# Kernel tuning notes

Measured on AMD Instinct MI355X. Metric: run time of the kernel, lower is better.

## Reference

```python
import jax, jax.numpy as jnp
import numpy as np

STRIDES = (8, 16, 32, 64, 128)
TOPK = 1000          # fixed candidate count (jit-friendly stand-in for boolean masking)
SCORE_TH = 0.05      # from `score > 0.05` in postProcessing
IOU_TH = 0.5         # standard FCOS NMS threshold


def _decode_level(cls, cnt, reg, stride):
    # cls [B,C,H,W], cnt [B,1,H,W], reg [B,4,H,W]
    B, C, H, W = cls.shape
    p_cls = jax.nn.sigmoid(cls).transpose(0, 2, 3, 1).reshape(B, H * W, C)
    p_cnt = jax.nn.sigmoid(cnt).transpose(0, 2, 3, 1).reshape(B, H * W, 1)
    p_reg = jnp.exp(reg).transpose(0, 2, 3, 1).reshape(B, H * W, 4)  # (l,t,r,b) distances
    ys = (jnp.arange(H, dtype=cls.dtype) + 0.5) * stride
    xs = (jnp.arange(W, dtype=cls.dtype) + 0.5) * stride
    yy, xx = jnp.meshgrid(ys, xs, indexing='ij')
    cx = xx.reshape(-1)[None, :]  # [1,HW]
    cy = yy.reshape(-1)[None, :]
    boxes = jnp.stack([cx - p_reg[..., 0], cy - p_reg[..., 1],
                       cx + p_reg[..., 2], cy + p_reg[..., 3]], axis=-1)  # [B,HW,4]
    return p_cls, p_cnt, boxes


def _iou_matrix(b):
    # b [K,4] (x1,y1,x2,y2) -> [K,K]
    area = jnp.clip(b[:, 2] - b[:, 0], 0) * jnp.clip(b[:, 3] - b[:, 1], 0)
    x1 = jnp.maximum(b[:, None, 0], b[None, :, 0])
    y1 = jnp.maximum(b[:, None, 1], b[None, :, 1])
    x2 = jnp.minimum(b[:, None, 2], b[None, :, 2])
    y2 = jnp.minimum(b[:, None, 3], b[None, :, 3])
    inter = jnp.clip(x2 - x1, 0) * jnp.clip(y2 - y1, 0)
    return inter / (area[:, None] + area[None, :] - inter + 1e-9)


def _nms_keep(boxes, scores):
    # boxes [K,4] sorted by descending score, scores [K] -> keep mask [K]
    K = boxes.shape[0]
    iou = _iou_matrix(boxes)
    idx = jnp.arange(K)
    keep0 = scores > SCORE_TH
    def body(i, keep):
        sup = (iou[i] > IOU_TH) & (idx > i) & keep[i]
        return keep & ~sup
    return jax.lax.fori_loop(0, K, body, keep0)


def _detect(levels):
    cls_l, cnt_l, box_l = [], [], []
    for (c, n, r), s in zip(levels, STRIDES):
        pc, pn, pb = _decode_level(c, n, r, s)
        cls_l.append(pc); cnt_l.append(pn); box_l.append(pb)
    cls = jnp.concatenate(cls_l, 1)    # [B,N,C]
    boxes = jnp.concatenate(box_l, 1)  # [B,N,4]
    score = cls.max(-1)                # per original: score from cls (cnt unused in score)
    kind = cls.argmax(-1)
    top_s, top_i = jax.lax.top_k(score, TOPK)                      # [B,K]
    top_b = jnp.take_along_axis(boxes, top_i[..., None], axis=1)   # [B,K,4]
    top_k = jnp.take_along_axis(kind, top_i, axis=1)               # [B,K]
    keep = jax.vmap(_nms_keep)(top_b, top_s)                       # [B,K] bool
    out = jnp.concatenate([top_b,
                           top_k[..., None].astype(cls.dtype),
                           top_s[..., None],
                           keep[..., None].astype(cls.dtype)], axis=-1)  # [B,K,7]
    return out


def setup_inputs() -> dict:
    key = jax.random.key(0)
    B, C = 16, 20
    hw = [(128, 160), (64, 80), (32, 40), (16, 20), (8, 10)]
    names = []
    for p in (3, 4, 5, 6, 7):
        names += [f'cls_p{p}', f'cnt_p{p}', f'reg_p{p}']
    ks = jax.random.split(key, len(names))
    inp = {}
    for li, (H, W) in enumerate(hw):
        inp[f'cls_p{li+3}'] = jax.random.normal(ks[3*li+0], (B, C, H, W), jnp.float32)
        inp[f'cnt_p{li+3}'] = jax.random.normal(ks[3*li+1], (B, 1, H, W), jnp.float32)
        inp[f'reg_p{li+3}'] = jax.random.normal(ks[3*li+2], (B, 4, H, W), jnp.float32)
    return inp


def reference(cls_p3, cnt_p3, reg_p3, cls_p4, cnt_p4, reg_p4,
              cls_p5, cnt_p5, reg_p5, cls_p6, cnt_p6, reg_p6,
              cls_p7, cnt_p7, reg_p7):
    levels = [(cls_p3, cnt_p3, reg_p3), (cls_p4, cnt_p4, reg_p4),
              (cls_p5, cnt_p5, reg_p5), (cls_p6, cnt_p6, reg_p6),
              (cls_p7, cnt_p7, reg_p7)]
    return _detect(levels)
```

## Files before the change

### kernel.cpp

```cpp
#include <hip/hip_runtime.h>
#include <math.h>

#define BATCH 16
#define NCH 20
#define NPOS 27280
#define NTOP 1000
#define KW 16
#define NBIN 4096
#define CANDCAP 4096

typedef unsigned long long u64;
typedef unsigned int u32;

__device__ __align__(16) u32 g_sb[BATCH * NPOS];
__device__ unsigned char g_kind[BATCH * NPOS];
__device__ float4 g_box[BATCH * NTOP];
__device__ float g_score[BATCH * NTOP];
__device__ u64 g_mask[BATCH * NTOP * KW];
__device__ unsigned char g_rowsup[BATCH * NTOP];

__device__ __forceinline__ int digit_of(u32 sb) {
  int d = ((int)sb - 0x3F000000) >> 11;
  return d < 0 ? 0 : (d > (NBIN - 1) ? (NBIN - 1) : d);
}

__device__ __forceinline__ int jj(int j) { return j + (j >> 6); }
#define SKEWCAP (NTOP + NTOP / 64 + 1)

__global__ __launch_bounds__(256) void k1_score(
    const float* __restrict__ c3, const float* __restrict__ c4,
    const float* __restrict__ c5, const float* __restrict__ c6,
    const float* __restrict__ c7) {
  int gid = blockIdx.x * 256 + threadIdx.x;
  if (gid >= BATCH * (NPOS / 4)) return;
  int b = gid / (NPOS / 4);
  int n0 = (gid - b * (NPOS / 4)) * 4;
  const float* cls; int off, hw;
  if (n0 < 20480)      { cls = c3; off = 0;     hw = 20480; }
  else if (n0 < 25600) { cls = c4; off = 20480; hw = 5120;  }
  else if (n0 < 26880) { cls = c5; off = 25600; hw = 1280;  }
  else if (n0 < 27200) { cls = c6; off = 26880; hw = 320;   }
  else                 { cls = c7; off = 27200; hw = 80;    }
  int local = n0 - off;
  const float4* p = (const float4*)(cls + (size_t)b * NCH * hw + local);
  int s4 = hw >> 2;
  float4 best = p[0];
  int k0 = 0, k1 = 0, k2 = 0, k3 = 0;
  for (int c = 1; c < NCH; ++c) {
    float4 v = p[(size_t)c * s4];
    if (v.x > best.x) { best.x = v.x; k0 = c; }
    if (v.y > best.y) { best.y = v.y; k1 = c; }
    if (v.z > best.z) { best.z = v.z; k2 = c; }
    if (v.w > best.w) { best.w = v.w; k3 = c; }
  }
  uint4 sb4;
  float bb[4] = {best.x, best.y, best.z, best.w};
  u32 sb[4];
#pragma unroll
  for (int i = 0; i < 4; ++i) {
    float e = (float)exp(-(double)bb[i]);
    float s = 1.0f / (1.0f + e);
    sb[i] = __float_as_uint(s);
  }
  sb4.x = sb[0]; sb4.y = sb[1]; sb4.z = sb[2]; sb4.w = sb[3];
  *(uint4*)&g_sb[(size_t)b * NPOS + n0] = sb4;
  u32 kind4 = (u32)k0 | ((u32)k1 << 8) | ((u32)k2 << 16) | ((u32)k3 << 24);
  *(u32*)&g_kind[(size_t)b * NPOS + n0] = kind4;
}

__global__ __launch_bounds__(1024) void k2_select(
    const float* __restrict__ r3, const float* __restrict__ r4,
    const float* __restrict__ r5, const float* __restrict__ r6,
    const float* __restrict__ r7, float* __restrict__ out) {
  int b = blockIdx.x;
  int tid = threadIdx.x;
  int lane = tid & 63, wid = tid >> 6;
  const u32* sbs = g_sb + (size_t)b * NPOS;

  __shared__ u32 arr[NBIN];
  __shared__ u32 suf[NBIN];
  __shared__ u64 scand[CANDCAP];
  __shared__ u32 wsum[16];
  __shared__ int sh_thr, sh_ncand;

  for (int j = tid; j < NBIN; j += 1024) arr[j] = 0;
  __syncthreads();

  for (int i = 0; i < 27; ++i) {
    int n = tid + i * 1024;
    if (n < NPOS) atomicAdd(&arr[digit_of(sbs[n])], 1u);
  }
  __syncthreads();

  {
    u32 c[4];
#pragma unroll
    for (int k = 0; k < 4; ++k) { c[k] = arr[4 * tid + k]; arr[4 * tid + k] = 0; }
    u32 tot = c[0] + c[1] + c[2] + c[3];
    u32 s = tot;
#pragma unroll
    for (int off = 1; off < 64; off <<= 1) {
      u32 v = __shfl_down(s, off);
      if (lane + off < 64) s += v;
    }
    if (lane == 0) wsum[wid] = s;
    __syncthreads();
    u32 wexcl = 0;
    for (int w2 = wid + 1; w2 < 16; ++w2) wexcl += wsum[w2];
    u32 e = wexcl + (s - tot);
    u32 e3 = e;
    u32 e2 = e3 + c[3];
    u32 e1 = e2 + c[2];
    u32 e0 = e1 + c[1];
    suf[4 * tid + 3] = e3;
    suf[4 * tid + 2] = e2;
    suf[4 * tid + 1] = e1;
    suf[4 * tid + 0] = e0;
    if (e3 < NTOP && NTOP <= e3 + c[3]) { sh_thr = 4 * tid + 3; sh_ncand = (int)(e3 + c[3]); }
    if (e2 < NTOP && NTOP <= e2 + c[2]) { sh_thr = 4 * tid + 2; sh_ncand = (int)(e2 + c[2]); }
    if (e1 < NTOP && NTOP <= e1 + c[1]) { sh_thr = 4 * tid + 1; sh_ncand = (int)(e1 + c[1]); }
    if (e0 < NTOP && NTOP <= e0 + c[0]) { sh_thr = 4 * tid + 0; sh_ncand = (int)(e0 + c[0]); }
  }
  __syncthreads();
  int thr = sh_thr;
  int Ncand = sh_ncand < CANDCAP ? sh_ncand : CANDCAP;

  for (int i = 0; i < 27; ++i) {
    int n = tid + i * 1024;
    if (n < NPOS) {
      u32 sb = sbs[n];
      int d = digit_of(sb);
      if (d >= thr) {
        u32 slot = suf[d] + atomicAdd(&arr[d], 1u);
        if (slot < CANDCAP) scand[slot] = ((u64)sb << 15) | (u32)(NPOS - n);
      }
    }
  }
  __syncthreads();

  for (int i = tid; i < Ncand; i += 1024) {
    u64 k = scand[i];
    int d = digit_of((u32)(k >> 15));
    u32 gs = suf[d];
    u32 ge = (d > 0) ? suf[d - 1] : (u32)NPOS;
    if (ge > (u32)Ncand) ge = (u32)Ncand;
    int rank = (int)gs;
    for (u32 j = gs; j < ge; ++j) rank += (int)(scand[j] > k);
    if (rank >= NTOP) continue;
    u32 n = (u32)NPOS - (u32)(k & 0x7FFFu);
    float sc = __uint_as_float((u32)(k >> 15));
    const float* reg; int off, hw, lvl;
    if (n < 20480)      { reg = r3; off = 0;     hw = 20480; lvl = 0; }
    else if (n < 25600) { reg = r4; off = 20480; hw = 5120;  lvl = 1; }
    else if (n < 26880) { reg = r5; off = 25600; hw = 1280;  lvl = 2; }
    else if (n < 27200) { reg = r6; off = 26880; hw = 320;   lvl = 3; }
    else                { reg = r7; off = 27200; hw = 80;    lvl = 4; }
    int local = (int)n - off;
    int W = 160 >> lvl;
    int hh = local / W, ww = local - hh * W;
    float stride = (float)(8 << lvl);
    const float* rp = reg + (size_t)b * 4 * hw + local;
    float e0 = expf(rp[0]);
    float e1 = expf(rp[(size_t)hw]);
    float e2 = expf(rp[(size_t)2 * hw]);
    float e3 = expf(rp[(size_t)3 * hw]);
    float cx = (ww + 0.5f) * stride, cy = (hh + 0.5f) * stride;
    float x1 = cx - e0, y1 = cy - e1, x2 = cx + e2, y2 = cy + e3;
    int ok = b * NTOP + rank;
    g_box[ok] = make_float4(x1, y1, x2, y2);
    g_score[ok] = sc;
    float* o = out + (size_t)ok * 7;
    o[0] = x1; o[1] = y1; o[2] = x2; o[3] = y2;
    o[4] = (float)g_kind[(size_t)b * NPOS + n];
    o[5] = sc;
  }
}

__global__ __launch_bounds__(256) void k3_mask() {
  int b = blockIdx.y;
  int ig = blockIdx.x;
  int tid = threadIdx.x;
  int lane = tid & 63;
  __shared__ float4 shbox[SKEWCAP];
  __shared__ float shA[SKEWCAP];
  const float4* boxes = g_box + b * NTOP;
  for (int j = tid; j < NTOP; j += 256) {
    float4 bj = boxes[j];
    shbox[jj(j)] = bj;
    shA[jj(j)] = fmaxf(bj.z - bj.x, 0.f) * fmaxf(bj.w - bj.y, 0.f);
  }
  __syncthreads();
  int i = ig * 16 + (tid >> 4);
  int t = tid & 15;
  u64 word = 0;
  if (i < NTOP) {
    float4 bi = shbox[jj(i)];
    float aarea = shA[jj(i)];
    int j0 = t * 64;
    int jbeg = (j0 > i + 1) ? j0 : i + 1;
    int jend = (j0 + 64 < NTOP) ? j0 + 64 : NTOP;
    for (int j = jbeg; j < jend; ++j) {
      float4 bj = shbox[jj(j)];
      float barea = shA[jj(j)];
      float ix1 = fmaxf(bi.x, bj.x), iy1 = fmaxf(bi.y, bj.y);
      float ix2 = fminf(bi.z, bj.z), iy2 = fminf(bi.w, bj.w);
      float inter = fmaxf(ix2 - ix1, 0.f) * fmaxf(iy2 - iy1, 0.f);
      if (inter + inter > aarea + barea - inter + 1e-9f)
        word |= 1ull << (j - j0);
    }
    g_mask[((size_t)b * NTOP + i) * KW + t] = word;
  }
  u64 b16 = __ballot(word != 0);
  int rg = lane >> 4;
  if (t == 0 && i < NTOP)
    g_rowsup[b * NTOP + i] = (unsigned char)(((b16 >> (rg * 16)) & 0xFFFFull) ? 1 : 0);
}

__global__ __launch_bounds__(64) void k4_greedy(float* __restrict__ out) {
  int b = blockIdx.x;
  int lane = threadIdx.x;
  int col = lane & 15, g = lane >> 4;
  const u64* mask = g_mask + (size_t)b * NTOP * KW;

  u64 mdiag[KW];
  float s[KW];
  unsigned char rs[KW];
#pragma unroll
  for (int w = 0; w < KW; ++w) {
    int k = w * 64 + lane;
    mdiag[w] = (k < NTOP) ? mask[(size_t)k * KW + w] : 0ull;
    s[w] = (k < NTOP) ? g_score[b * NTOP + k] : 0.f;
    rs[w] = (k < NTOP) ? g_rowsup[b * NTOP + k] : (unsigned char)0;
  }

  u64 remv = 0;
  for (int w = 0; w < KW; ++w) {
    int k = w * 64 + lane;
    u64 keep0 = __ballot(k < NTOP && s[w] > 0.05f);
    u64 gate = __ballot(rs[w] != 0);
    u64 cur = keep0 & ~__shfl(remv, w);
    u64 rem = cur & gate;
    u64 acc = 0;
    while (rem) {
      int i = __ffsll(rem) - 1;
      u64 v = __shfl(mdiag[w], i);
      rem &= ~(v | (1ull << i));
      cur &= ~v;
      acc |= (1ull << i);
    }
    u64 upd = 0;
#pragma unroll
    for (int r = 0; r < 16; ++r) {
      int i2 = g * 16 + r;
      if ((acc >> i2) & 1ull)
        upd |= mask[(size_t)(w * 64 + i2) * KW + col];
    }
    upd |= __shfl_xor(upd, 16);
    upd |= __shfl_xor(upd, 32);
    remv |= upd;
    if (k < NTOP) out[(size_t)(b * NTOP + k) * 7 + 6] = (float)((cur >> lane) & 1ull);
  }
}

extern "C" void kernel_launch(void* const* d_in, const int* in_sizes, int n_in,
                              void* d_out, int out_size, void* d_ws, size_t ws_size,
                              hipStream_t stream) {
  const float* c3 = (const float*)d_in[0];
  const float* r3 = (const float*)d_in[2];
  const float* c4 = (const float*)d_in[3];
  const float* r4 = (const float*)d_in[5];
  const float* c5 = (const float*)d_in[6];
  const float* r5 = (const float*)d_in[8];
  const float* c6 = (const float*)d_in[9];
  const float* r6 = (const float*)d_in[11];
  const float* c7 = (const float*)d_in[12];
  const float* r7 = (const float*)d_in[14];
  float* out = (float*)d_out;

  int total4 = BATCH * (NPOS / 4);
  hipLaunchKernelGGL(k1_score, dim3((total4 + 255) / 256), dim3(256), 0, stream,
                     c3, c4, c5, c6, c7);
  hipLaunchKernelGGL(k2_select, dim3(BATCH), dim3(1024), 0, stream,
                     r3, r4, r5, r6, r7, out);
  hipLaunchKernelGGL(k3_mask, dim3(63, BATCH), dim3(256), 0, stream);
  hipLaunchKernelGGL(k4_greedy, dim3(BATCH), dim3(64), 0, stream, out);
}
```

Measured before the change: 64.31 us.

## Split top-k selection into histogram, scan, compact and rank kernels across slices

The per-batch single-block select kernel is broken up. Score histograms are now built per slice inside the score kernel, then merged and scanned in a separate kernel, and candidates are compacted by a grid of blocks into a global buffer before a ranking kernel runs. The mask kernel also loads only the boxes from its row group onward into shared memory. The aim is to spread the histogram and compaction work across many blocks instead of 16 large blocks, at the cost of two more launches and of global-memory atomics and candidate storage in place of shared memory.

```diff
diff --git a/kernel.cpp b/kernel.cpp
--- a/kernel.cpp
+++ b/kernel.cpp
@@ -8,12 +8,20 @@
 #define KW 16
 #define NBIN 4096
 #define CANDCAP 4096
+#define NSLICE 7
 
 typedef unsigned long long u64;
 typedef unsigned int u32;
 
 __device__ __align__(16) u32 g_sb[BATCH * NPOS];
 __device__ unsigned char g_kind[BATCH * NPOS];
+__device__ u32 g_hph[BATCH * NSLICE * NBIN];
+__device__ u32 g_suf[BATCH * NBIN];
+__device__ u32 g_cnt[BATCH * NBIN];
+__device__ u32 g_dcnt[BATCH * NBIN];
+__device__ int g_thr[BATCH];
+__device__ int g_ncand[BATCH];
+__device__ u64 g_cand[BATCH * CANDCAP];
 __device__ float4 g_box[BATCH * NTOP];
 __device__ float g_score[BATCH * NTOP];
 __device__ u64 g_mask[BATCH * NTOP * KW];
@@ -27,125 +35,127 @@
 __device__ __forceinline__ int jj(int j) { return j + (j >> 6); }
 #define SKEWCAP (NTOP + NTOP / 64 + 1)
 
-__global__ __launch_bounds__(256) void k1_score(
+__global__ __launch_bounds__(1024) void k1_score(
     const float* __restrict__ c3, const float* __restrict__ c4,
     const float* __restrict__ c5, const float* __restrict__ c6,
     const float* __restrict__ c7) {
-  int gid = blockIdx.x * 256 + threadIdx.x;
-  if (gid >= BATCH * (NPOS / 4)) return;
-  int b = gid / (NPOS / 4);
-  int n0 = (gid - b * (NPOS / 4)) * 4;
-  const float* cls; int off, hw;
-  if (n0 < 20480)      { cls = c3; off = 0;     hw = 20480; }
-  else if (n0 < 25600) { cls = c4; off = 20480; hw = 5120;  }
-  else if (n0 < 26880) { cls = c5; off = 25600; hw = 1280;  }
-  else if (n0 < 27200) { cls = c6; off = 26880; hw = 320;   }
-  else                 { cls = c7; off = 27200; hw = 80;    }
-  int local = n0 - off;
-  const float4* p = (const float4*)(cls + (size_t)b * NCH * hw + local);
-  int s4 = hw >> 2;
-  float4 best = p[0];
-  int k0 = 0, k1 = 0, k2 = 0, k3 = 0;
-  for (int c = 1; c < NCH; ++c) {
-    float4 v = p[(size_t)c * s4];
-    if (v.x > best.x) { best.x = v.x; k0 = c; }
-    if (v.y > best.y) { best.y = v.y; k1 = c; }
-    if (v.z > best.z) { best.z = v.z; k2 = c; }
-    if (v.w > best.w) { best.w = v.w; k3 = c; }
-  }
-  uint4 sb4;
-  float bb[4] = {best.x, best.y, best.z, best.w};
-  u32 sb[4];
+  int b = blockIdx.y, bx = blockIdx.x, tid = threadIdx.x;
+  __shared__ u32 lh[NBIN];
+  for (int j = tid; j < NBIN; j += 1024) lh[j] = 0;
+  __syncthreads();
+
+  int n0 = bx * 4096 + tid * 4;
+  if (n0 < NPOS) {
+    const float* cls; int off, hw;
+    if (n0 < 20480)      { cls = c3; off = 0;     hw = 20480; }
+    else if (n0 < 25600) { cls = c4; off = 20480; hw = 5120;  }
+    else if (n0 < 26880) { cls = c5; off = 25600; hw = 1280;  }
+    else if (n0 < 27200) { cls = c6; off = 26880; hw = 320;   }
+    else                 { cls = c7; off = 27200; hw = 80;    }
+    int local = n0 - off;
+    const float4* p = (const float4*)(cls + (size_t)b * NCH * hw + local);
+    int s4 = hw >> 2;
+    float4 best = p[0];
+    int k0 = 0, k1 = 0, k2 = 0, k3 = 0;
+    for (int c = 1; c < NCH; ++c) {
+      float4 v = p[(size_t)c * s4];
+      if (v.x > best.x) { best.x = v.x; k0 = c; }
+      if (v.y > best.y) { best.y = v.y; k1 = c; }
+      if (v.z > best.z) { best.z = v.z; k2 = c; }
+      if (v.w > best.w) { best.w = v.w; k3 = c; }
+    }
+    float bb[4] = {best.x, best.y, best.z, best.w};
+    u32 sb[4];
+#pragma unroll
+    for (int i = 0; i < 4; ++i) {
+      float e = (float)exp(-(double)bb[i]);
+      float s = 1.0f / (1.0f + e);
+      sb[i] = __float_as_uint(s);
+      atomicAdd(&lh[digit_of(sb[i])], 1u);
+    }
+    uint4 sb4; sb4.x = sb[0]; sb4.y = sb[1]; sb4.z = sb[2]; sb4.w = sb[3];
+    *(uint4*)&g_sb[(size_t)b * NPOS + n0] = sb4;
+    u32 kind4 = (u32)k0 | ((u32)k1 << 8) | ((u32)k2 << 16) | ((u32)k3 << 24);
+    *(u32*)&g_kind[(size_t)b * NPOS + n0] = kind4;
+  }
+  __syncthreads();
+  u32* ph = g_hph + ((size_t)b * NSLICE + bx) * NBIN;
+  for (int j = tid; j < NBIN; j += 1024) ph[j] = lh[j];
+}
+
+__global__ __launch_bounds__(1024) void k2_scan() {
+  int b = blockIdx.x, tid = threadIdx.x;
+  int lane = tid & 63, wid = tid >> 6;
+  __shared__ u32 wsum[16];
+  u32 c[4];
+#pragma unroll
+  for (int k = 0; k < 4; ++k) {
+    int d = 4 * tid + k;
+    u32 s = 0;
+    for (int p = 0; p < NSLICE; ++p) s += g_hph[((size_t)b * NSLICE + p) * NBIN + d];
+    c[k] = s;
+    g_cnt[b * NBIN + d] = s;
+  }
+  u32 tot = c[0] + c[1] + c[2] + c[3];
+  u32 s = tot;
+#pragma unroll
+  for (int off = 1; off < 64; off <<= 1) {
+    u32 v = __shfl_down(s, off);
+    if (lane + off < 64) s += v;
+  }
+  if (lane == 0) wsum[wid] = s;
+  __syncthreads();
+  u32 wexcl = 0;
+  for (int w2 = wid + 1; w2 < 16; ++w2) wexcl += wsum[w2];
+  u32 e = wexcl + (s - tot);
+  u32 e3 = e;
+  u32 e2 = e3 + c[3];
+  u32 e1 = e2 + c[2];
+  u32 e0 = e1 + c[1];
+  g_suf[b * NBIN + 4 * tid + 3] = e3;
+  g_suf[b * NBIN + 4 * tid + 2] = e2;
+  g_suf[b * NBIN + 4 * tid + 1] = e1;
+  g_suf[b * NBIN + 4 * tid + 0] = e0;
+  if (e3 < NTOP && NTOP <= e3 + c[3]) { g_thr[b] = 4 * tid + 3; g_ncand[b] = (int)(e3 + c[3]); }
+  if (e2 < NTOP && NTOP <= e2 + c[2]) { g_thr[b] = 4 * tid + 2; g_ncand[b] = (int)(e2 + c[2]); }
+  if (e1 < NTOP && NTOP <= e1 + c[1]) { g_thr[b] = 4 * tid + 1; g_ncand[b] = (int)(e1 + c[1]); }
+  if (e0 < NTOP && NTOP <= e0 + c[0]) { g_thr[b] = 4 * tid + 0; g_ncand[b] = (int)(e0 + c[0]); }
+  for (int j = tid; j < NBIN; j += 1024) g_dcnt[b * NBIN + j] = 0;
+}
+
+__global__ __launch_bounds__(1024) void k3_compact() {
+  int b = blockIdx.y, bx = blockIdx.x, tid = threadIdx.x;
+  int n0 = bx * 4096 + tid * 4;
+  if (n0 >= NPOS) return;
+  int thr = g_thr[b];
+  uint4 sb4 = *(const uint4*)&g_sb[(size_t)b * NPOS + n0];
+  u32 sb[4] = {sb4.x, sb4.y, sb4.z, sb4.w};
 #pragma unroll
   for (int i = 0; i < 4; ++i) {
-    float e = (float)exp(-(double)bb[i]);
-    float s = 1.0f / (1.0f + e);
-    sb[i] = __float_as_uint(s);
-  }
-  sb4.x = sb[0]; sb4.y = sb[1]; sb4.z = sb[2]; sb4.w = sb[3];
-  *(uint4*)&g_sb[(size_t)b * NPOS + n0] = sb4;
-  u32 kind4 = (u32)k0 | ((u32)k1 << 8) | ((u32)k2 << 16) | ((u32)k3 << 24);
-  *(u32*)&g_kind[(size_t)b * NPOS + n0] = kind4;
-}
-
-__global__ __launch_bounds__(1024) void k2_select(
+    int d = digit_of(sb[i]);
+    if (d >= thr) {
+      u32 slot = g_suf[b * NBIN + d] + atomicAdd(&g_dcnt[b * NBIN + d], 1u);
+      if (slot < CANDCAP)
+        g_cand[b * CANDCAP + slot] = ((u64)sb[i] << 15) | (u32)(NPOS - (n0 + i));
+    }
+  }
+}
+
+__global__ __launch_bounds__(1024) void k4_rank(
     const float* __restrict__ r3, const float* __restrict__ r4,
     const float* __restrict__ r5, const float* __restrict__ r6,
     const float* __restrict__ r7, float* __restrict__ out) {
-  int b = blockIdx.x;
-  int tid = threadIdx.x;
-  int lane = tid & 63, wid = tid >> 6;
-  const u32* sbs = g_sb + (size_t)b * NPOS;
-
-  __shared__ u32 arr[NBIN];
-  __shared__ u32 suf[NBIN];
-  __shared__ u64 scand[CANDCAP];
-  __shared__ u32 wsum[16];
-  __shared__ int sh_thr, sh_ncand;
-
-  for (int j = tid; j < NBIN; j += 1024) arr[j] = 0;
-  __syncthreads();
-
-  for (int i = 0; i < 27; ++i) {
-    int n = tid + i * 1024;
-    if (n < NPOS) atomicAdd(&arr[digit_of(sbs[n])], 1u);
-  }
-  __syncthreads();
-
-  {
-    u32 c[4];
-#pragma unroll
-    for (int k = 0; k < 4; ++k) { c[k] = arr[4 * tid + k]; arr[4 * tid + k] = 0; }
-    u32 tot = c[0] + c[1] + c[2] + c[3];
-    u32 s = tot;
-#pragma unroll
-    for (int off = 1; off < 64; off <<= 1) {
-      u32 v = __shfl_down(s, off);
-      if (lane + off < 64) s += v;
-    }
-    if (lane == 0) wsum[wid] = s;
-    __syncthreads();
-    u32 wexcl = 0;
-    for (int w2 = wid + 1; w2 < 16; ++w2) wexcl += wsum[w2];
-    u32 e = wexcl + (s - tot);
-    u32 e3 = e;
-    u32 e2 = e3 + c[3];
-    u32 e1 = e2 + c[2];
-    u32 e0 = e1 + c[1];
-    suf[4 * tid + 3] = e3;
-    suf[4 * tid + 2] = e2;
-    suf[4 * tid + 1] = e1;
-    suf[4 * tid + 0] = e0;
-    if (e3 < NTOP && NTOP <= e3 + c[3]) { sh_thr = 4 * tid + 3; sh_ncand = (int)(e3 + c[3]); }
-    if (e2 < NTOP && NTOP <= e2 + c[2]) { sh_thr = 4 * tid + 2; sh_ncand = (int)(e2 + c[2]); }
-    if (e1 < NTOP && NTOP <= e1 + c[1]) { sh_thr = 4 * tid + 1; sh_ncand = (int)(e1 + c[1]); }
-    if (e0 < NTOP && NTOP <= e0 + c[0]) { sh_thr = 4 * tid + 0; sh_ncand = (int)(e0 + c[0]); }
-  }
-  __syncthreads();
-  int thr = sh_thr;
-  int Ncand = sh_ncand < CANDCAP ? sh_ncand : CANDCAP;
-
-  for (int i = 0; i < 27; ++i) {
-    int n = tid + i * 1024;
-    if (n < NPOS) {
-      u32 sb = sbs[n];
-      int d = digit_of(sb);
-      if (d >= thr) {
-        u32 slot = suf[d] + atomicAdd(&arr[d], 1u);
-        if (slot < CANDCAP) scand[slot] = ((u64)sb << 15) | (u32)(NPOS - n);
-      }
-    }
-  }
-  __syncthreads();
-
-  for (int i = tid; i < Ncand; i += 1024) {
-    u64 k = scand[i];
+  int b = blockIdx.x, tid = threadIdx.x;
+  int ncand = g_ncand[b];
+  if (ncand > CANDCAP) ncand = CANDCAP;
+  for (int i = tid; i < ncand; i += 1024) {
+    u64 k = g_cand[b * CANDCAP + i];
     int d = digit_of((u32)(k >> 15));
-    u32 gs = suf[d];
-    u32 ge = (d > 0) ? suf[d - 1] : (u32)NPOS;
-    if (ge > (u32)Ncand) ge = (u32)Ncand;
+    u32 gs = g_suf[b * NBIN + d];
+    u32 ge = gs + g_cnt[b * NBIN + d];
+    if (ge > (u32)ncand) ge = (u32)ncand;
     int rank = (int)gs;
-    for (u32 j = gs; j < ge; ++j) rank += (int)(scand[j] > k);
+    for (u32 j = gs; j < ge; ++j) rank += (int)(g_cand[b * CANDCAP + j] > k);
     if (rank >= NTOP) continue;
     u32 n = (u32)NPOS - (u32)(k & 0x7FFFu);
     float sc = __uint_as_float((u32)(k >> 15));
@@ -176,32 +186,34 @@
   }
 }
 
-__global__ __launch_bounds__(256) void k3_mask() {
+__global__ __launch_bounds__(256) void k5_mask() {
   int b = blockIdx.y;
   int ig = blockIdx.x;
   int tid = threadIdx.x;
   int lane = tid & 63;
+  int jlo = ig * 16;
+  int nst = NTOP - jlo;
   __shared__ float4 shbox[SKEWCAP];
   __shared__ float shA[SKEWCAP];
   const float4* boxes = g_box + b * NTOP;
-  for (int j = tid; j < NTOP; j += 256) {
-    float4 bj = boxes[j];
+  for (int j = tid; j < nst; j += 256) {
+    float4 bj = boxes[jlo + j];
     shbox[jj(j)] = bj;
     shA[jj(j)] = fmaxf(bj.z - bj.x, 0.f) * fmaxf(bj.w - bj.y, 0.f);
   }
   __syncthreads();
-  int i = ig * 16 + (tid >> 4);
+  int i = jlo + (tid >> 4);
   int t = tid & 15;
   u64 word = 0;
   if (i < NTOP) {
-    float4 bi = shbox[jj(i)];
-    float aarea = shA[jj(i)];
+    float4 bi = shbox[jj(i - jlo)];
+    float aarea = shA[jj(i - jlo)];
     int j0 = t * 64;
     int jbeg = (j0 > i + 1) ? j0 : i + 1;
     int jend = (j0 + 64 < NTOP) ? j0 + 64 : NTOP;
     for (int j = jbeg; j < jend; ++j) {
-      float4 bj = shbox[jj(j)];
-      float barea = shA[jj(j)];
+      float4 bj = shbox[jj(j - jlo)];
+      float barea = shA[jj(j - jlo)];
       float ix1 = fmaxf(bi.x, bj.x), iy1 = fmaxf(bi.y, bj.y);
       float ix2 = fminf(bi.z, bj.z), iy2 = fminf(bi.w, bj.w);
       float inter = fmaxf(ix2 - ix1, 0.f) * fmaxf(iy2 - iy1, 0.f);
@@ -216,7 +228,7 @@
     g_rowsup[b * NTOP + i] = (unsigned char)(((b16 >> (rg * 16)) & 0xFFFFull) ? 1 : 0);
 }
 
-__global__ __launch_bounds__(64) void k4_greedy(float* __restrict__ out) {
+__global__ __launch_bounds__(64) void k6_greedy(float* __restrict__ out) {
   int b = blockIdx.x;
   int lane = threadIdx.x;
   int col = lane & 15, g = lane >> 4;
@@ -277,11 +289,12 @@
   const float* r7 = (const float*)d_in[14];
   float* out = (float*)d_out;
 
-  int total4 = BATCH * (NPOS / 4);
-  hipLaunchKernelGGL(k1_score, dim3((total4 + 255) / 256), dim3(256), 0, stream,
+  hipLaunchKernelGGL(k1_score, dim3(NSLICE, BATCH), dim3(1024), 0, stream,
                      c3, c4, c5, c6, c7);
-  hipLaunchKernelGGL(k2_select, dim3(BATCH), dim3(1024), 0, stream,
+  hipLaunchKernelGGL(k2_scan, dim3(BATCH), dim3(1024), 0, stream);
+  hipLaunchKernelGGL(k3_compact, dim3(NSLICE, BATCH), dim3(1024), 0, stream);
+  hipLaunchKernelGGL(k4_rank, dim3(BATCH), dim3(1024), 0, stream,
                      r3, r4, r5, r6, r7, out);
-  hipLaunchKernelGGL(k3_mask, dim3(63, BATCH), dim3(256), 0, stream);
-  hipLaunchKernelGGL(k4_greedy, dim3(BATCH), dim3(64), 0, stream, out);
-}
+  hipLaunchKernelGGL(k5_mask, dim3(63, BATCH), dim3(256), 0, stream);
+  hipLaunchKernelGGL(k6_greedy, dim3(BATCH), dim3(64), 0, stream, out);
+}
```

Result: no change. 63.08 us (-1.9%).
